# Kernel optimization log

Hardware: AMD Instinct MI355X
Metric: run time of the kernel (lower is better)

## Reference

```python
import jax, jax.numpy as jnp
import numpy as np

N, E, D, H = 50000, 400000, 128, 256


def setup_inputs() -> dict:
    key = jax.random.key(0)
    ks = jax.random.split(key, 16)
    s = 0.02
    inp = {
        "x": jax.random.normal(ks[0], (N, D), dtype=jnp.float32),
        "edge_index": jax.random.randint(ks[1], (2, E), 0, N, dtype=jnp.int64),
        "steps": 1,
        # encoder MLP: Linear(D->H), Linear(H->H), relu after each
        "enc_w1": jax.random.normal(ks[2], (H, D), dtype=jnp.float32) * s,
        "enc_b1": jnp.zeros((H,), dtype=jnp.float32),
        "enc_w2": jax.random.normal(ks[3], (H, H), dtype=jnp.float32) * s,
        "enc_b2": jnp.zeros((H,), dtype=jnp.float32),
        # GeneralConv lin_msg (root_weight=False, bias=True)
        "msg_w": jax.random.normal(ks[4], (H, H), dtype=jnp.float32) * s,
        "msg_b": jnp.zeros((H,), dtype=jnp.float32),
        # decoder MLP: Linear(2H->H) relu, Linear(H->D) tanh
        "dec_w1": jax.random.normal(ks[5], (H, 2 * H), dtype=jnp.float32) * s,
        "dec_b1": jnp.zeros((H,), dtype=jnp.float32),
        "dec_w2": jax.random.normal(ks[6], (D, H), dtype=jnp.float32) * s,
        "dec_b2": jnp.zeros((D,), dtype=jnp.float32),
    }
    return inp


def reference(x, edge_index, steps, enc_w1, enc_b1, enc_w2, enc_b2,
              msg_w, msg_b, dec_w1, dec_b1, dec_w2, dec_b2):
    src = edge_index[0]
    dst = edge_index[1]
    n = x.shape[0]
    for _ in range(steps):  # steps is a small static python int
        # encoder MLP (batch_norm=False, dropout=0, relu + relu)
        h = jax.nn.relu(x @ enc_w1.T + enc_b1)
        h = jax.nn.relu(h @ enc_w2.T + enc_b2)
        # GeneralConv: message = lin_msg(x_j); aggr='add'; no root weight
        # lin_msg is edge-independent -> transform on nodes, then gather/scatter
        m = h @ msg_w.T + msg_b                      # [N, H]
        out = jax.ops.segment_sum(m[src], dst, num_segments=n)  # [N, H]
        # decoder on cat(out, h): relu then tanh
        d = jax.nn.relu(jnp.concatenate([out, h], axis=-1) @ dec_w1.T + dec_b1)
        x = jnp.tanh(d @ dec_w2.T + dec_b2)
    return x
```

## Files before the change

kernel.cpp:

```cpp
#include <hip/hip_runtime.h>
#include <cmath>


typedef __attribute__((ext_vector_type(8))) short  short8;
typedef __attribute__((ext_vector_type(4))) float  f32x4;
typedef __attribute__((ext_vector_type(4))) unsigned short us4;

typedef unsigned short u16;
typedef unsigned int   u32;

static __device__ __forceinline__ u16 f2bf(float f) {
    u32 u = __float_as_uint(f);
    u = (u + 0x7FFFu + ((u >> 16) & 1u)) >> 16;
    return (u16)u;
}
static __device__ __forceinline__ float bf2f(u16 h) {
    return __uint_as_float(((u32)h) << 16);
}

static __device__ __forceinline__ void g2l16(const void* g, void* l) {
    __builtin_amdgcn_global_load_lds(
        (const __attribute__((address_space(1))) u32*)g,
        (__attribute__((address_space(3))) u32*)l, 16, 0, 0);
}

template <int ACT, bool OUT_BF16>
__global__ __launch_bounds__(256) void gemm_bf16(
    const u16* __restrict__ A0, const u16* __restrict__ A1,
    const int K0, const int K,
    const u16* __restrict__ W, const float* __restrict__ bias,
    void* __restrict__ Cout, const int N, const int M)
{
    __shared__ u16 As[128 * 64];
    __shared__ u16 Ws[128 * 64];

    const int t    = threadIdx.x;
    const int c0   = blockIdx.x * 128;
    const int r0   = blockIdx.y * 128;
    const int wave = t >> 6;
    const int lane = t & 63;
    const int n    = lane & 15;
    const int q    = lane >> 4;
    const int wr   = (wave & 1) * 64;
    const int wc   = (wave >> 1) * 64;

    const int lrow = lane >> 3;
    const int qofs = (lane & 7) * 8;

    const int KA1 = K - K0;
    const u16 *a0p[4], *a1p[4], *wp[4];
    u16 *ldsA[4], *ldsW[4];
#pragma unroll
    for (int k2 = 0; k2 < 4; k2++) {
        const int g    = wave + k2 * 4;
        const int grow = g * 8 + lrow;
        const int arow = min(r0 + grow, N - 1);
        a0p[k2] = A0 + (size_t)arow * K0 + qofs;
        a1p[k2] = A1 + (size_t)arow * KA1 + qofs;
        wp[k2]  = W + (size_t)(c0 + grow) * K + qofs;
        ldsA[k2] = &As[g * 512];
        ldsW[k2] = &Ws[g * 512];
    }

    f32x4 acc[4][4];
#pragma unroll
    for (int i = 0; i < 4; i++)
#pragma unroll
        for (int j = 0; j < 4; j++) acc[i][j] = (f32x4)0.0f;

    for (int kc = 0; kc < K; kc += 64) {
        __syncthreads();
        if (kc < K0) {
#pragma unroll
            for (int k2 = 0; k2 < 4; k2++) g2l16(a0p[k2] + kc, ldsA[k2]);
        } else {
#pragma unroll
            for (int k2 = 0; k2 < 4; k2++) g2l16(a1p[k2] + (kc - K0), ldsA[k2]);
        }
#pragma unroll
        for (int k2 = 0; k2 < 4; k2++) g2l16(wp[k2] + kc, ldsW[k2]);
        __syncthreads();

#pragma unroll
        for (int h = 0; h < 2; h++) {
            short8 af[4], bf[4];
#pragma unroll
            for (int i = 0; i < 4; i++)
                af[i] = *reinterpret_cast<const short8*>(
                    &As[(wr + i * 16 + n) * 64 + h * 32 + q * 8]);
#pragma unroll
            for (int j = 0; j < 4; j++)
                bf[j] = *reinterpret_cast<const short8*>(
                    &Ws[(wc + j * 16 + n) * 64 + h * 32 + q * 8]);
#pragma unroll
            for (int i = 0; i < 4; i++)
#pragma unroll
                for (int j = 0; j < 4; j++)
                    acc[i][j] = __builtin_amdgcn_mfma_f32_16x16x32_bf16(
                        af[i], bf[j], acc[i][j], 0, 0, 0);
        }
    }

    float bv[4];
#pragma unroll
    for (int j = 0; j < 4; j++) bv[j] = bias[c0 + wc + j * 16 + n];

#pragma unroll
    for (int i = 0; i < 4; i++) {
        const int rbase = r0 + wr + i * 16 + q * 4;
#pragma unroll
        for (int reg = 0; reg < 4; reg++) {
            const int row = rbase + reg;
            if (row < N) {
#pragma unroll
                for (int j = 0; j < 4; j++) {
                    const int col = c0 + wc + j * 16 + n;
                    float v = acc[i][j][reg] + bv[j];
                    if (ACT == 1) v = fmaxf(v, 0.0f);
                    if (ACT == 2) v = tanhf(v);
                    if (OUT_BF16)
                        ((u16*)Cout)[(size_t)row * M + col] = f2bf(v);
                    else
                        ((float*)Cout)[(size_t)row * M + col] = v;
                }
            }
        }
    }
}

__global__ __launch_bounds__(256) void cvt_kernel(
    const float* __restrict__ s, u16* __restrict__ d, const int n4)
{
    const int i = blockIdx.x * 256 + threadIdx.x;
    if (i < n4) {
        const float4 v = reinterpret_cast<const float4*>(s)[i];
        us4 o = { f2bf(v.x), f2bf(v.y), f2bf(v.z), f2bf(v.w) };
        reinterpret_cast<us4*>(d)[i] = o;
    }
}

__global__ __launch_bounds__(256) void cvt5_kernel(
    const float* s0, const float* s1, const float* s2, const float* s3,
    const float* s4, u16* d0, u16* d1, u16* d2, u16* d3, u16* d4,
    int n0, int n1, int n2, int n3, int n4)
{
    const float* s; u16* d; int n4c;
    switch (blockIdx.y) {
        case 0: s = s0; d = d0; n4c = n0; break;
        case 1: s = s1; d = d1; n4c = n1; break;
        case 2: s = s2; d = d2; n4c = n2; break;
        case 3: s = s3; d = d3; n4c = n3; break;
        default: s = s4; d = d4; n4c = n4; break;
    }
    const int i = blockIdx.x * 256 + threadIdx.x;
    if (i < n4c) {
        const float4 v = reinterpret_cast<const float4*>(s)[i];
        us4 o = { f2bf(v.x), f2bf(v.y), f2bf(v.z), f2bf(v.w) };
        reinterpret_cast<us4*>(d)[i] = o;
    }
}

__global__ __launch_bounds__(256) void zero_kernel(
    int* __restrict__ p, const int n)
{
    const int i = blockIdx.x * 256 + threadIdx.x;
    if (i < n) p[i] = 0;
}

__global__ __launch_bounds__(256) void histo_kernel(
    const int* __restrict__ ei, int* __restrict__ deg, const int E,
    const int Nn)
{
    const int e = blockIdx.x * 256 + threadIdx.x;
    if (e < E) {
        const int dst = ei[(size_t)E + e];
        if ((unsigned)dst < (unsigned)Nn) atomicAdd(&deg[dst], 1);
    }
}

__global__ __launch_bounds__(256) void scan_reduce_kernel(
    const int* __restrict__ deg, int* __restrict__ bsums, const int Nn)
{
    __shared__ int s[256];
    const int t = threadIdx.x;
    const int i = blockIdx.x * 256 + t;
    s[t] = (i < Nn) ? deg[i] : 0;
    __syncthreads();
    for (int d = 128; d > 0; d >>= 1) {
        if (t < d) s[t] += s[t + d];
        __syncthreads();
    }
    if (t == 0) bsums[blockIdx.x] = s[0];
}

__global__ __launch_bounds__(256) void scan_sums_kernel(
    const int* __restrict__ bsums, int* __restrict__ bscan, const int nb)
{
    __shared__ int s[256];
    const int t = threadIdx.x;
    const int v = (t < nb) ? bsums[t] : 0;
    s[t] = v;
    __syncthreads();
    for (int d = 1; d < 256; d <<= 1) {
        int u = (t >= d) ? s[t - d] : 0;
        __syncthreads();
        s[t] += u;
        __syncthreads();
    }
    if (t < nb) bscan[t] = s[t] - v;
}

__global__ __launch_bounds__(256) void scan_final_kernel(
    const int* __restrict__ deg, const int* __restrict__ bscan,
    int* __restrict__ offsets, int* __restrict__ cursor, const int Nn)
{
    __shared__ int s[256];
    const int t = threadIdx.x;
    const int i = blockIdx.x * 256 + t;
    const int v = (i < Nn) ? deg[i] : 0;
    s[t] = v;
    __syncthreads();
    for (int d = 1; d < 256; d <<= 1) {
        int u = (t >= d) ? s[t - d] : 0;
        __syncthreads();
        s[t] += u;
        __syncthreads();
    }
    const int excl = s[t] - v + bscan[blockIdx.x];
    if (i < Nn) {
        offsets[i] = excl;
        cursor[i]  = excl;
        if (i == Nn - 1) offsets[Nn] = excl + v;
    }
}

__global__ __launch_bounds__(256) void fill_kernel(
    const int* __restrict__ ei, int* __restrict__ cursor,
    int* __restrict__ bucket, const int E, const int Nn)
{
    const int e = blockIdx.x * 256 + threadIdx.x;
    if (e < E) {
        const int src = ei[e];
        const int dst = ei[(size_t)E + e];
        if ((unsigned)dst < (unsigned)Nn) {
            const int pos = atomicAdd(&cursor[dst], 1);
            if ((unsigned)pos < (unsigned)E) bucket[pos] = src;
        }
    }
}

__global__ __launch_bounds__(256) void gather_sum_kernel(
    const u16* __restrict__ m, const int* __restrict__ bucket,
    const int* __restrict__ offsets, u16* __restrict__ out,
    const int Nn, const int E)
{
    const int wave = (int)((blockIdx.x * 256u + threadIdx.x) >> 6);
    const int lane = threadIdx.x & 63;
    if (wave >= Nn) return;
    int beg = offsets[wave];
    int end = offsets[wave + 1];
    beg = max(0, min(beg, E));
    end = max(beg, min(end, E));
    float a0 = 0.f, a1 = 0.f, a2 = 0.f, a3 = 0.f;
    int e = beg;
    for (; e + 3 < end; e += 4) {
        int sidx[4];
#pragma unroll
        for (int u = 0; u < 4; u++) sidx[u] = bucket[e + u];
        us4 v[4];
#pragma unroll
        for (int u = 0; u < 4; u++) {
            const int s = ((unsigned)sidx[u] < (unsigned)Nn) ? sidx[u] : 0;
            v[u] = *reinterpret_cast<const us4*>(&m[(size_t)s * 256 + lane * 4]);
        }
#pragma unroll
        for (int u = 0; u < 4; u++) {
            if ((unsigned)sidx[u] < (unsigned)Nn) {
                a0 += bf2f(v[u].x); a1 += bf2f(v[u].y);
                a2 += bf2f(v[u].z); a3 += bf2f(v[u].w);
            }
        }
    }
    for (; e < end; e++) {
        const int s0 = bucket[e];
        if ((unsigned)s0 < (unsigned)Nn) {
            const us4 v0 = *reinterpret_cast<const us4*>(
                &m[(size_t)s0 * 256 + lane * 4]);
            a0 += bf2f(v0.x); a1 += bf2f(v0.y);
            a2 += bf2f(v0.z); a3 += bf2f(v0.w);
        }
    }
    us4 o = { f2bf(a0), f2bf(a1), f2bf(a2), f2bf(a3) };
    *reinterpret_cast<us4*>(&out[(size_t)wave * 256 + lane * 4]) = o;
}

extern "C" void kernel_launch(void* const* d_in, const int* in_sizes, int n_in,
                              void* d_out, int out_size, void* d_ws, size_t ws_size,
                              hipStream_t stream)
{
    const float* x      = (const float*)d_in[0];
    const int*   ei     = (const int*)d_in[1];
    const float* enc_w1 = (const float*)d_in[3];
    const float* enc_b1 = (const float*)d_in[4];
    const float* enc_w2 = (const float*)d_in[5];
    const float* enc_b2 = (const float*)d_in[6];
    const float* msg_w  = (const float*)d_in[7];
    const float* msg_b  = (const float*)d_in[8];
    const float* dec_w1 = (const float*)d_in[9];
    const float* dec_b1 = (const float*)d_in[10];
    const float* dec_w2 = (const float*)d_in[11];
    const float* dec_b2 = (const float*)d_in[12];

    const int N = 50000, D = 128, H = 256;
    const int E = in_sizes[1] / 2;
    const int NB = (N + 255) / 256;

    u16* xb   = (u16*)d_ws;
    u16* h1   = xb   + (size_t)N * D;
    u16* h    = h1   + (size_t)N * H;
    u16* m    = h    + (size_t)N * H;
    u16* aggr = m    + (size_t)N * H;
    u16* dbuf = aggr + (size_t)N * H;
    u16* w_enc1 = dbuf + (size_t)N * H;
    u16* w_enc2 = w_enc1 + 256 * 128;
    u16* w_msg  = w_enc2 + 256 * 256;
    u16* w_dec1 = w_msg  + 256 * 256;
    u16* w_dec2 = w_dec1 + 256 * 512;
    int* deg     = (int*)(w_dec2 + 128 * 256);
    int* offsets = deg + N;
    int* cursor  = offsets + N + 1;
    int* bucket  = cursor + N;
    int* bsums   = bucket + E;
    int* bscan   = bsums + NB;

    const dim3 blk(256);
    const dim3 gridH(2, (N + 127) / 128);
    const dim3 gridD(1, (N + 127) / 128);
    const int eblk = (E + 255) / 256;

    cvt_kernel<<<dim3((N * D / 4 + 255) / 256), blk, 0, stream>>>(x, xb, N * D / 4);
    cvt5_kernel<<<dim3((256 * 512 / 4 + 255) / 256, 5), blk, 0, stream>>>(
        enc_w1, enc_w2, msg_w, dec_w1, dec_w2,
        w_enc1, w_enc2, w_msg, w_dec1, w_dec2,
        256 * 128 / 4, 256 * 256 / 4, 256 * 256 / 4, 256 * 512 / 4, 128 * 256 / 4);

    zero_kernel<<<dim3(NB), blk, 0, stream>>>(deg, N);
    histo_kernel<<<dim3(eblk), blk, 0, stream>>>(ei, deg, E, N);
    scan_reduce_kernel<<<dim3(NB), blk, 0, stream>>>(deg, bsums, N);
    scan_sums_kernel<<<dim3(1), blk, 0, stream>>>(bsums, bscan, NB);
    scan_final_kernel<<<dim3(NB), blk, 0, stream>>>(deg, bscan, offsets,
                                                    cursor, N);
    fill_kernel<<<dim3(eblk), blk, 0, stream>>>(ei, cursor, bucket, E, N);

    gemm_bf16<1, true><<<gridH, blk, 0, stream>>>(xb, xb, D, D, w_enc1, enc_b1,
                                                  h1, N, H);
    gemm_bf16<1, true><<<gridH, blk, 0, stream>>>(h1, h1, H, H, w_enc2, enc_b2,
                                                  h, N, H);
    gemm_bf16<0, true><<<gridH, blk, 0, stream>>>(h, h, H, H, w_msg, msg_b,
                                                  m, N, H);
    gather_sum_kernel<<<dim3((N * 64 + 255) / 256), blk, 0, stream>>>(
        m, bucket, offsets, aggr, N, E);
    gemm_bf16<1, true><<<gridH, blk, 0, stream>>>(aggr, h, H, 2 * H, w_dec1,
                                                  dec_b1, dbuf, N, H);
    gemm_bf16<2, false><<<gridD, blk, 0, stream>>>(dbuf, dbuf, H, H, w_dec2,
                                                   dec_b2, (float*)d_out, N, D);
}
```

Before: 284.9 us.

## Double-buffer GEMM LDS tiles with K=32 steps and merge conversion launches

The bf16 GEMM now uses two LDS buffers with 32-wide K tiles. It prefetches the next tile via global_load_lds while MFMAs run on the current one, and needs one barrier per step instead of two. The x conversion is folded into the weight-conversion kernel, saving one launch. The trade-off is more loop iterations and barriers per K, and the merged kernel launches many idle blocks for the small weight slices. The single barrier placed before the prefetch looks like it may race with reads of the other buffer, so correctness depends on the ordering holding.

```diff
diff --git a/kernel.cpp b/kernel.cpp
--- a/kernel.cpp
+++ b/kernel.cpp
@@ -31,8 +31,8 @@
     const u16* __restrict__ W, const float* __restrict__ bias,
     void* __restrict__ Cout, const int N, const int M)
 {
-    __shared__ u16 As[128 * 64];
-    __shared__ u16 Ws[128 * 64];
+    __shared__ u16 As[2][128 * 32];
+    __shared__ u16 Ws[2][128 * 32];
 
     const int t    = threadIdx.x;
     const int c0   = blockIdx.x * 128;
@@ -44,23 +44,19 @@
     const int wr   = (wave & 1) * 64;
     const int wc   = (wave >> 1) * 64;
 
-    const int lrow = lane >> 3;
-    const int qofs = (lane & 7) * 8;
+    const int grow0 = wave * 16 + (lane >> 2);
+    const int grow1 = (wave + 4) * 16 + (lane >> 2);
+    const int qofs  = (lane & 3) * 8;
 
     const int KA1 = K - K0;
-    const u16 *a0p[4], *a1p[4], *wp[4];
-    u16 *ldsA[4], *ldsW[4];
-#pragma unroll
-    for (int k2 = 0; k2 < 4; k2++) {
-        const int g    = wave + k2 * 4;
-        const int grow = g * 8 + lrow;
-        const int arow = min(r0 + grow, N - 1);
-        a0p[k2] = A0 + (size_t)arow * K0 + qofs;
-        a1p[k2] = A1 + (size_t)arow * KA1 + qofs;
-        wp[k2]  = W + (size_t)(c0 + grow) * K + qofs;
-        ldsA[k2] = &As[g * 512];
-        ldsW[k2] = &Ws[g * 512];
-    }
+    const int ar0 = min(r0 + grow0, N - 1);
+    const int ar1 = min(r0 + grow1, N - 1);
+    const u16* a0b0 = A0 + (size_t)ar0 * K0 + qofs;
+    const u16* a0b1 = A0 + (size_t)ar1 * K0 + qofs;
+    const u16* a1b0 = A1 + (size_t)ar0 * KA1 + qofs;
+    const u16* a1b1 = A1 + (size_t)ar1 * KA1 + qofs;
+    const u16* wb0  = W + (size_t)(c0 + grow0) * K + qofs;
+    const u16* wb1  = W + (size_t)(c0 + grow1) * K + qofs;
 
     f32x4 acc[4][4];
 #pragma unroll
@@ -68,37 +64,51 @@
 #pragma unroll
         for (int j = 0; j < 4; j++) acc[i][j] = (f32x4)0.0f;
 
-    for (int kc = 0; kc < K; kc += 64) {
-        __syncthreads();
-        if (kc < K0) {
-#pragma unroll
-            for (int k2 = 0; k2 < 4; k2++) g2l16(a0p[k2] + kc, ldsA[k2]);
+    {
+        if (0 < K0) {
+            g2l16(a0b0, &As[0][wave * 512]);
+            g2l16(a0b1, &As[0][(wave + 4) * 512]);
         } else {
-#pragma unroll
-            for (int k2 = 0; k2 < 4; k2++) g2l16(a1p[k2] + (kc - K0), ldsA[k2]);
-        }
-#pragma unroll
-        for (int k2 = 0; k2 < 4; k2++) g2l16(wp[k2] + kc, ldsW[k2]);
-        __syncthreads();
-
-#pragma unroll
-        for (int h = 0; h < 2; h++) {
-            short8 af[4], bf[4];
-#pragma unroll
-            for (int i = 0; i < 4; i++)
-                af[i] = *reinterpret_cast<const short8*>(
-                    &As[(wr + i * 16 + n) * 64 + h * 32 + q * 8]);
+            g2l16(a1b0, &As[0][wave * 512]);
+            g2l16(a1b1, &As[0][(wave + 4) * 512]);
+        }
+        g2l16(wb0, &Ws[0][wave * 512]);
+        g2l16(wb1, &Ws[0][(wave + 4) * 512]);
+    }
+
+    int buf = 0;
+    for (int kc = 0; kc < K; kc += 32) {
+        __syncthreads();
+        const int kn = kc + 32;
+        if (kn < K) {
+            const int nb = buf ^ 1;
+            if (kn < K0) {
+                g2l16(a0b0 + kn, &As[nb][wave * 512]);
+                g2l16(a0b1 + kn, &As[nb][(wave + 4) * 512]);
+            } else {
+                g2l16(a1b0 + (kn - K0), &As[nb][wave * 512]);
+                g2l16(a1b1 + (kn - K0), &As[nb][(wave + 4) * 512]);
+            }
+            g2l16(wb0 + kn, &Ws[nb][wave * 512]);
+            g2l16(wb1 + kn, &Ws[nb][(wave + 4) * 512]);
+        }
+
+        short8 af[4], bf[4];
+#pragma unroll
+        for (int i = 0; i < 4; i++)
+            af[i] = *reinterpret_cast<const short8*>(
+                &As[buf][(wr + i * 16 + n) * 32 + q * 8]);
+#pragma unroll
+        for (int j = 0; j < 4; j++)
+            bf[j] = *reinterpret_cast<const short8*>(
+                &Ws[buf][(wc + j * 16 + n) * 32 + q * 8]);
+#pragma unroll
+        for (int i = 0; i < 4; i++)
 #pragma unroll
             for (int j = 0; j < 4; j++)
-                bf[j] = *reinterpret_cast<const short8*>(
-                    &Ws[(wc + j * 16 + n) * 64 + h * 32 + q * 8]);
-#pragma unroll
-            for (int i = 0; i < 4; i++)
-#pragma unroll
-                for (int j = 0; j < 4; j++)
-                    acc[i][j] = __builtin_amdgcn_mfma_f32_16x16x32_bf16(
-                        af[i], bf[j], acc[i][j], 0, 0, 0);
-        }
+                acc[i][j] = __builtin_amdgcn_mfma_f32_16x16x32_bf16(
+                    af[i], bf[j], acc[i][j], 0, 0, 0);
+        buf ^= 1;
     }
 
     float bv[4];
@@ -128,32 +138,23 @@
     }
 }
 
-__global__ __launch_bounds__(256) void cvt_kernel(
-    const float* __restrict__ s, u16* __restrict__ d, const int n4)
-{
+__global__ __launch_bounds__(256) void cvt6_kernel(
+    const float* s0, const float* s1, const float* s2, const float* s3,
+    const float* s4, const float* s5,
+    u16* d0, u16* d1, u16* d2, u16* d3, u16* d4, u16* d5,
+    int n0, int n1, int n2, int n3, int n4, int n5)
+{
+    const float* s; u16* d; int nq;
+    switch (blockIdx.y) {
+        case 0: s = s0; d = d0; nq = n0; break;
+        case 1: s = s1; d = d1; nq = n1; break;
+        case 2: s = s2; d = d2; nq = n2; break;
+        case 3: s = s3; d = d3; nq = n3; break;
+        case 4: s = s4; d = d4; nq = n4; break;
+        default: s = s5; d = d5; nq = n5; break;
+    }
     const int i = blockIdx.x * 256 + threadIdx.x;
-    if (i < n4) {
-        const float4 v = reinterpret_cast<const float4*>(s)[i];
-        us4 o = { f2bf(v.x), f2bf(v.y), f2bf(v.z), f2bf(v.w) };
-        reinterpret_cast<us4*>(d)[i] = o;
-    }
-}
-
-__global__ __launch_bounds__(256) void cvt5_kernel(
-    const float* s0, const float* s1, const float* s2, const float* s3,
-    const float* s4, u16* d0, u16* d1, u16* d2, u16* d3, u16* d4,
-    int n0, int n1, int n2, int n3, int n4)
-{
-    const float* s; u16* d; int n4c;
-    switch (blockIdx.y) {
-        case 0: s = s0; d = d0; n4c = n0; break;
-        case 1: s = s1; d = d1; n4c = n1; break;
-        case 2: s = s2; d = d2; n4c = n2; break;
-        case 3: s = s3; d = d3; n4c = n3; break;
-        default: s = s4; d = d4; n4c = n4; break;
-    }
-    const int i = blockIdx.x * 256 + threadIdx.x;
-    if (i < n4c) {
+    if (i < nq) {
         const float4 v = reinterpret_cast<const float4*>(s)[i];
         us4 o = { f2bf(v.x), f2bf(v.y), f2bf(v.z), f2bf(v.w) };
         reinterpret_cast<us4*>(d)[i] = o;
@@ -338,11 +339,11 @@
     const dim3 gridD(1, (N + 127) / 128);
     const int eblk = (E + 255) / 256;
 
-    cvt_kernel<<<dim3((N * D / 4 + 255) / 256), blk, 0, stream>>>(x, xb, N * D / 4);
-    cvt5_kernel<<<dim3((256 * 512 / 4 + 255) / 256, 5), blk, 0, stream>>>(
-        enc_w1, enc_w2, msg_w, dec_w1, dec_w2,
-        w_enc1, w_enc2, w_msg, w_dec1, w_dec2,
-        256 * 128 / 4, 256 * 256 / 4, 256 * 256 / 4, 256 * 512 / 4, 128 * 256 / 4);
+    cvt6_kernel<<<dim3((N * D / 4 + 255) / 256, 6), blk, 0, stream>>>(
+        x, enc_w1, enc_w2, msg_w, dec_w1, dec_w2,
+        xb, w_enc1, w_enc2, w_msg, w_dec1, w_dec2,
+        N * D / 4, 256 * 128 / 4, 256 * 256 / 4, 256 * 256 / 4,
+        256 * 512 / 4, 128 * 256 / 4);
 
     zero_kernel<<<dim3(NB), blk, 0, stream>>>(deg, N);
     histo_kernel<<<dim3(eblk), blk, 0, stream>>>(ei, deg, E, N);
```

Measured after the change: 299.9 us. 5.3% more time.
